# Performance work log

Hardware: AMD Instinct MI355X
Metric: run time of the kernel (lower is better)

The kernel has to match this reference:

```python
import jax, jax.numpy as jnp
import numpy as np

EMBED_DIM = 1024
NUM_HEADS = 16
HEAD_DIM = EMBED_DIM // NUM_HEADS
B, T = 4, 2048


def setup_inputs() -> dict:
    key = jax.random.key(0)
    ks = jax.random.split(key, 5)
    s = 0.02
    return {
        "x": jax.random.normal(ks[0], (B, T, EMBED_DIM), dtype=jnp.float32),
        "qkv_w": jax.random.normal(ks[1], (3 * EMBED_DIM, EMBED_DIM), dtype=jnp.float32) * s,
        "qkv_b": jax.random.normal(ks[2], (3 * EMBED_DIM,), dtype=jnp.float32) * s,
        "out_w": jax.random.normal(ks[3], (EMBED_DIM, EMBED_DIM), dtype=jnp.float32) * s,
        "out_b": jax.random.normal(ks[4], (EMBED_DIM,), dtype=jnp.float32) * s,
    }


def reference(x, qkv_w, qkv_b, out_w, out_b):
    b, t, c = x.shape
    h, d = NUM_HEADS, HEAD_DIM
    # qkv projection: Linear uses y = x @ W^T + b
    qkv = jnp.einsum("btc,fc->btf", x, qkv_w) + qkv_b  # [B,T,3C]
    q, k, v = jnp.split(qkv, 3, axis=-1)
    # [B, H, T, D]
    q = q.reshape(b, t, h, d).transpose(0, 2, 1, 3)
    k = k.reshape(b, t, h, d).transpose(0, 2, 1, 3)
    v = v.reshape(b, t, h, d).transpose(0, 2, 1, 3)
    scores = jnp.einsum("bhqd,bhkd->bhqk", q, k) / jnp.sqrt(jnp.float32(d))
    causal = jnp.tril(jnp.ones((t, t), dtype=bool))
    scores = jnp.where(causal, scores, -jnp.inf)
    attn = jax.nn.softmax(scores, axis=-1)
    o = jnp.einsum("bhqk,bhkd->bhqd", attn, v)
    o = o.transpose(0, 2, 1, 3).reshape(b, t, c)
    return jnp.einsum("btc,fc->btf", o, out_w) + out_b
```

## Files before the change

kernel.cpp:

```cpp
#include <hip/hip_runtime.h>
#include <hip/hip_bf16.h>
#include <math.h>

#define SEQ   2048
#define NTOK  8192
#define EMB   1024
#define QKVF  3072
#define QSCALE 0.18033688f

typedef __bf16 bf16;
typedef __bf16 bf16x8 __attribute__((ext_vector_type(8)));
typedef __bf16 bf16x4 __attribute__((ext_vector_type(4)));
typedef unsigned short u16x8 __attribute__((ext_vector_type(8)));
typedef float  f32x4  __attribute__((ext_vector_type(4)));

__device__ __forceinline__ void gload_lds16(const bf16* g, bf16* l) {
    __builtin_amdgcn_global_load_lds(
        (const __attribute__((address_space(1))) unsigned int*)g,
        (__attribute__((address_space(3))) unsigned int*)l,
        16, 0, 0);
}

__global__ __launch_bounds__(256) void cvt_f32_bf16(const float* __restrict__ in,
                                                    bf16* __restrict__ out, int n) {
    int i = (blockIdx.x * 256 + threadIdx.x) * 4;
    if (i >= n) return;
    float4 f = *reinterpret_cast<const float4*>(in + i);
    bf16x4 o;
    o[0] = (bf16)f.x; o[1] = (bf16)f.y; o[2] = (bf16)f.z; o[3] = (bf16)f.w;
    *reinterpret_cast<bf16x4*>(out + i) = o;
}

__global__ __launch_bounds__(256) void cvt_qkvw_bf16(const float* __restrict__ in,
                                                     bf16* __restrict__ out) {
    int i = (blockIdx.x * 256 + threadIdx.x) * 4;
    float4 f = *reinterpret_cast<const float4*>(in + i);
    const float s = (i < EMB * EMB) ? QSCALE : 1.f;
    bf16x4 o;
    o[0] = (bf16)(f.x * s); o[1] = (bf16)(f.y * s);
    o[2] = (bf16)(f.z * s); o[3] = (bf16)(f.w * s);
    *reinterpret_cast<bf16x4*>(out + i) = o;
}

template <bool BF16OUT>
__global__ __launch_bounds__(256) void gemm_bt(const bf16* __restrict__ A,
                                               const bf16* __restrict__ Bm,
                                               const float* __restrict__ bias,
                                               void* __restrict__ out,
                                               int M, int N, int K, int scale_cols) {
    __shared__ bf16 As[2][128 * 64];
    __shared__ bf16 Bs[2][128 * 64];

    const int nbx = N >> 7;
    const int q8  = (nbx * (M >> 7)) >> 3;
    const int swz = ((int)blockIdx.x & 7) * q8 + ((int)blockIdx.x >> 3);
    const int bx  = swz % nbx;
    const int by  = swz / nbx;

    const int tid  = threadIdx.x;
    const int lane = tid & 63;
    const int wv   = tid >> 6;
    const int wr   = wv >> 1, wc = wv & 1;
    const int lr   = lane & 15, hi = lane >> 4;
    const size_t brow = (size_t)by * 128;
    const size_t bcol = (size_t)bx * 128;

    const f32x4 fzero = {0.f, 0.f, 0.f, 0.f};
    f32x4 acc[4][4];
#pragma unroll
    for (int m = 0; m < 4; ++m)
#pragma unroll
        for (int n = 0; n < 4; ++n) acc[m][n] = fzero;

    const int r8 = tid >> 3;
    const int c8 = tid & 7;

#define STAGE(buf, kt) do {                                                     \
    _Pragma("unroll")                                                           \
    for (int i_ = 0; i_ < 4; ++i_) {                                            \
        const int row_ = i_ * 32 + r8;                                          \
        const int lin_ = i_ * 256 + tid;                                        \
        gload_lds16(A  + (brow + row_) * (size_t)K + (size_t)(kt) * 64 + c8*8,  \
                    &As[buf][lin_ * 8]);                                        \
        gload_lds16(Bm + (bcol + row_) * (size_t)K + (size_t)(kt) * 64 + c8*8,  \
                    &Bs[buf][lin_ * 8]);                                        \
    }                                                                           \
} while (0)

    const int NT = K >> 6;
    STAGE(0, 0);
    int cur = 0;

    for (int kt = 0; kt < NT; ++kt) {
        if (kt + 1 < NT) {
            STAGE(cur ^ 1, kt + 1);
            asm volatile("s_waitcnt vmcnt(8)" ::: "memory");
        } else {
            asm volatile("s_waitcnt vmcnt(0)" ::: "memory");
        }
        __builtin_amdgcn_s_barrier();

#pragma unroll
        for (int kk = 0; kk < 2; ++kk) {
            bf16x8 af[4], bfr[4];
#pragma unroll
            for (int m = 0; m < 4; ++m)
                af[m] = *reinterpret_cast<const bf16x8*>(
                    &As[cur][(wr * 64 + m * 16 + lr) * 64 + kk * 32 + hi * 8]);
#pragma unroll
            for (int n = 0; n < 4; ++n)
                bfr[n] = *reinterpret_cast<const bf16x8*>(
                    &Bs[cur][(wc * 64 + n * 16 + lr) * 64 + kk * 32 + hi * 8]);
#pragma unroll
            for (int m = 0; m < 4; ++m)
#pragma unroll
                for (int n = 0; n < 4; ++n)
                    acc[m][n] = __builtin_amdgcn_mfma_f32_16x16x32_bf16(
                        af[m], bfr[n], acc[m][n], 0, 0, 0);
        }

        asm volatile("s_waitcnt lgkmcnt(0)" ::: "memory");
        __builtin_amdgcn_s_barrier();
        cur ^= 1;
    }

#pragma unroll
    for (int m = 0; m < 4; ++m)
#pragma unroll
        for (int n = 0; n < 4; ++n)
#pragma unroll
            for (int r = 0; r < 4; ++r) {
                const size_t row = brow + wr * 64 + m * 16 + hi * 4 + r;
                const size_t col = bcol + wc * 64 + n * 16 + lr;
                const float bb = bias[col];
                const float v = acc[m][n][r] + (((int)col < scale_cols) ? bb * QSCALE : bb);
                if (BF16OUT)
                    ((bf16*)out)[row * (size_t)N + col] = (bf16)v;
                else
                    ((float*)out)[row * (size_t)N + col] = v;
            }
#undef STAGE
}

__global__ __launch_bounds__(256) void attn_kernel(const bf16* __restrict__ qkv,
                                                   bf16* __restrict__ o) {
    const int bid = blockIdx.x;
    const int qt  = 15 - (bid >> 6);
    const int bh  = bid & 63;
    const int h   = bh & 15;
    const int b   = bh >> 4;
    const int qbase = qt * 128;

    const int tid  = threadIdx.x;
    const int wv   = tid >> 6;
    const int lane = tid & 63;
    const int lr   = lane & 15, hi = lane >> 4;

    __shared__ bf16 Ks[64 * 64];
    __shared__ bf16 Vt[64 * 64];
    __shared__ bf16 Pl[4 * 32 * 64];

    char* Ksb = (char*)Ks;
    char* Vtb = (char*)Vt;
    char* Pb  = (char*)(Pl + wv * 2048);

    const size_t tokbase = (size_t)b * SEQ;

    bf16x8 aq[2][2];
#pragma unroll
    for (int qf = 0; qf < 2; ++qf) {
        const bf16* qg = qkv + (tokbase + qbase + wv * 32 + qf * 16 + lr) * (size_t)QKVF
                         + h * 64;
#pragma unroll
        for (int kk = 0; kk < 2; ++kk)
            aq[qf][kk] = *reinterpret_cast<const bf16x8*>(qg + kk * 32 + hi * 8);
    }

    const f32x4 fzero = {0.f, 0.f, 0.f, 0.f};
    f32x4 oacc[2][4];
#pragma unroll
    for (int qf = 0; qf < 2; ++qf)
#pragma unroll
        for (int n = 0; n < 4; ++n) oacc[qf][n] = fzero;
    float m_r[2] = {-__builtin_inff(), -__builtin_inff()};
    float l_r[2] = {0.f, 0.f};

    const int nkv = qt * 2 + 2;

    const int kp = tid >> 3;
    const int vc = tid & 7;

    for (int kt = 0; kt < nkv; ++kt) {
        const size_t kvrow = tokbase + (size_t)kt * 64;
        __syncthreads();

#pragma unroll
        for (int j = 0; j < 2; ++j) {
            const int kr = wv * 16 + j * 8 + (lane >> 3);
            const int cg = (lane & 7) ^ ((lane >> 3) & 7);
            gload_lds16(qkv + (kvrow + kr) * (size_t)QKVF + EMB + h * 64 + cg * 8,
                        &Ks[(wv * 16 + j * 8) * 64 + lane * 8]);
        }

        {
            const bf16* vg = qkv + (kvrow + 2 * kp) * (size_t)QKVF + 2 * EMB + h * 64 + vc * 8;
            u16x8 v0 = *reinterpret_cast<const u16x8*>(vg);
            u16x8 v1 = *reinterpret_cast<const u16x8*>(vg + QKVF);
#pragma unroll
            for (int jj = 0; jj < 8; ++jj) {
                const int d = vc * 8 + jj;
                const unsigned int pr = (unsigned int)v0[jj] | ((unsigned int)v1[jj] << 16);
                *(unsigned int*)(Vtb + d * 128 + ((4 * kp) ^ (vc << 4))) = pr;
            }
        }
        __syncthreads();

        f32x4 s[2][4];
#pragma unroll
        for (int qf = 0; qf < 2; ++qf)
#pragma unroll
            for (int ktile = 0; ktile < 4; ++ktile) s[qf][ktile] = fzero;
#pragma unroll
        for (int ktile = 0; ktile < 4; ++ktile)
#pragma unroll
            for (int kk = 0; kk < 2; ++kk) {
                const int kr = ktile * 16 + lr;
                bf16x8 ak = *reinterpret_cast<const bf16x8*>(
                    Ksb + kr * 128 + ((kk * 64 + hi * 16) ^ ((kr & 7) << 4)));
#pragma unroll
                for (int qf = 0; qf < 2; ++qf)
                    s[qf][ktile] = __builtin_amdgcn_mfma_f32_16x16x32_bf16(
                        ak, aq[qf][kk], s[qf][ktile], 0, 0, 0);
            }

#pragma unroll
        for (int qf = 0; qf < 2; ++qf) {
            if (kt * 64 + 63 > qbase + wv * 32 + qf * 16) {
                const int qglob = qbase + wv * 32 + qf * 16 + lr;
#pragma unroll
                for (int ktile = 0; ktile < 4; ++ktile) {
                    const int kg0 = kt * 64 + ktile * 16 + hi * 4;
#pragma unroll
                    for (int r = 0; r < 4; ++r)
                        if (kg0 + r > qglob) s[qf][ktile][r] = -__builtin_inff();
                }
            }
        }

#pragma unroll
        for (int qf = 0; qf < 2; ++qf) {
            float t4[4];
#pragma unroll
            for (int ktile = 0; ktile < 4; ++ktile)
                t4[ktile] = fmaxf(fmaxf(s[qf][ktile][0], s[qf][ktile][1]),
                                  fmaxf(s[qf][ktile][2], s[qf][ktile][3]));
            float tm = fmaxf(fmaxf(t4[0], t4[1]), fmaxf(t4[2], t4[3]));
            tm = fmaxf(tm, __shfl_xor(tm, 16));
            tm = fmaxf(tm, __shfl_xor(tm, 32));

            const float mn = fmaxf(m_r[qf], tm);
            const float sc = __builtin_amdgcn_exp2f(m_r[qf] - mn);
            m_r[qf] = mn;

            float s4[4];
#pragma unroll
            for (int ktile = 0; ktile < 4; ++ktile) {
                float p0 = __builtin_amdgcn_exp2f(s[qf][ktile][0] - mn);
                float p1 = __builtin_amdgcn_exp2f(s[qf][ktile][1] - mn);
                float p2 = __builtin_amdgcn_exp2f(s[qf][ktile][2] - mn);
                float p3 = __builtin_amdgcn_exp2f(s[qf][ktile][3] - mn);
                s[qf][ktile][0] = p0; s[qf][ktile][1] = p1;
                s[qf][ktile][2] = p2; s[qf][ktile][3] = p3;
                s4[ktile] = (p0 + p1) + (p2 + p3);
            }
            float ts = (s4[0] + s4[1]) + (s4[2] + s4[3]);
            ts += __shfl_xor(ts, 16);
            ts += __shfl_xor(ts, 32);
            l_r[qf] = l_r[qf] * sc + ts;

            float scb[4];
#pragma unroll
            for (int r = 0; r < 4; ++r) scb[r] = __shfl(sc, hi * 4 + r);
#pragma unroll
            for (int n = 0; n < 4; ++n)
#pragma unroll
                for (int r = 0; r < 4; ++r) oacc[qf][n][r] *= scb[r];

            const int q = qf * 16 + lr;
#pragma unroll
            for (int ktile = 0; ktile < 4; ++ktile) {
                bf16x4 p4;
#pragma unroll
                for (int r = 0; r < 4; ++r) p4[r] = (bf16)s[qf][ktile][r];
                *(bf16x4*)(Pb + q * 128 + ((ktile * 32 + hi * 8) ^ ((q & 7) << 4))) = p4;
            }
        }

#pragma unroll
        for (int kk = 0; kk < 2; ++kk) {
            bf16x8 ap[2];
#pragma unroll
            for (int qf = 0; qf < 2; ++qf) {
                const int q = qf * 16 + lr;
                ap[qf] = *reinterpret_cast<const bf16x8*>(
                    Pb + q * 128 + ((kk * 64 + hi * 16) ^ ((q & 7) << 4)));
            }
#pragma unroll
            for (int n = 0; n < 4; ++n) {
                const int d = n * 16 + lr;
                bf16x8 bv = *reinterpret_cast<const bf16x8*>(
                    Vtb + d * 128 + ((kk * 64 + hi * 16) ^ (((d >> 3) & 7) << 4)));
#pragma unroll
                for (int qf = 0; qf < 2; ++qf)
                    oacc[qf][n] = __builtin_amdgcn_mfma_f32_16x16x32_bf16(
                        ap[qf], bv, oacc[qf][n], 0, 0, 0);
            }
        }
    }

#pragma unroll
    for (int qf = 0; qf < 2; ++qf) {
        const float linv = 1.f / l_r[qf];
        float li[4];
#pragma unroll
        for (int r = 0; r < 4; ++r) li[r] = __shfl(linv, hi * 4 + r);
        bf16* og = o + (tokbase + qbase + wv * 32 + qf * 16) * (size_t)EMB + h * 64;
#pragma unroll
        for (int n = 0; n < 4; ++n)
#pragma unroll
            for (int r = 0; r < 4; ++r)
                og[(hi * 4 + r) * (size_t)EMB + n * 16 + lr] =
                    (bf16)(oacc[qf][n][r] * li[r]);
    }
}

extern "C" void kernel_launch(void* const* d_in, const int* in_sizes, int n_in,
                              void* d_out, int out_size, void* d_ws, size_t ws_size,
                              hipStream_t stream) {
    const float* x     = (const float*)d_in[0];
    const float* qkv_w = (const float*)d_in[1];
    const float* qkv_b = (const float*)d_in[2];
    const float* out_w = (const float*)d_in[3];
    const float* out_b = (const float*)d_in[4];
    float* out = (float*)d_out;

    char* ws = (char*)d_ws;
    bf16* x_bf    = (bf16*)(ws);
    bf16* qkvw_bf = (bf16*)(ws + 16777216);
    bf16* outw_bf = (bf16*)(ws + 23068672);
    bf16* qkv_bf  = (bf16*)(ws + 25165824);
    bf16* o_bf    = (bf16*)(ws + 75497472);

    cvt_f32_bf16<<<8192, 256, 0, stream>>>(x,     x_bf,    NTOK * EMB);
    cvt_qkvw_bf16<<<3072, 256, 0, stream>>>(qkv_w, qkvw_bf);
    cvt_f32_bf16<<<1024, 256, 0, stream>>>(out_w, outw_bf, EMB * EMB);

    gemm_bt<true><<<(QKVF / 128) * (NTOK / 128), 256, 0, stream>>>(
        x_bf, qkvw_bf, qkv_b, qkv_bf, NTOK, QKVF, EMB, EMB);

    attn_kernel<<<4 * 16 * (SEQ / 128), 256, 0, stream>>>(qkv_bf, o_bf);

    gemm_bt<false><<<(EMB / 128) * (NTOK / 128), 256, 0, stream>>>(
        o_bf, outw_bf, out_b, out, NTOK, EMB, EMB, 0);
}
```

Measured before the change: 292.7 us.

## Enlarge GEMM tiles to 8 waves, swizzle LDS, shrink attention query tiles, defer rescale

The GEMM becomes a templated 512-thread kernel with 128x256 or 256x128 tiles, an XOR-swizzled LDS layout that avoids bank conflicts, and raised wave priority around the MFMA block. The attention kernel now uses 64-query tiles with one 16-row fragment per wave, which doubles the block count for better balance across the causal triangle. It also skips the online-softmax rescale of the output accumulator when no row's max increases. Larger GEMM tiles cut operand refetch but use more LDS and registers per block. Smaller attention tiles mean each K/V tile loaded into LDS is reused by fewer queries.

```diff
diff --git a/kernel.cpp b/kernel.cpp
--- a/kernel.cpp
+++ b/kernel.cpp
@@ -42,28 +42,30 @@
     *reinterpret_cast<bf16x4*>(out + i) = o;
 }
 
-template <bool BF16OUT>
-__global__ __launch_bounds__(256) void gemm_bt(const bf16* __restrict__ A,
-                                               const bf16* __restrict__ Bm,
-                                               const float* __restrict__ bias,
-                                               void* __restrict__ out,
-                                               int M, int N, int K, int scale_cols) {
-    __shared__ bf16 As[2][128 * 64];
-    __shared__ bf16 Bs[2][128 * 64];
-
-    const int nbx = N >> 7;
-    const int q8  = (nbx * (M >> 7)) >> 3;
+template <int WR, int WC, bool BF16OUT>
+__global__ __launch_bounds__(512, 2) void gemm_bt8(const bf16* __restrict__ A,
+                                                   const bf16* __restrict__ Bm,
+                                                   const float* __restrict__ bias,
+                                                   void* __restrict__ out,
+                                                   int M, int N, int K, int scale_cols) {
+    constexpr int BM = WR * 64, BN = WC * 64;
+    constexpr int WN = WR + WC;
+    __shared__ bf16 As[2][BM * 64];
+    __shared__ bf16 Bs[2][BN * 64];
+
+    const int nbx = N / BN;
+    const int q8  = (nbx * (M / BM)) >> 3;
     const int swz = ((int)blockIdx.x & 7) * q8 + ((int)blockIdx.x >> 3);
     const int bx  = swz % nbx;
     const int by  = swz / nbx;
 
     const int tid  = threadIdx.x;
     const int lane = tid & 63;
-    const int wv   = tid >> 6;
-    const int wr   = wv >> 1, wc = wv & 1;
+    const int wid  = tid >> 6;
+    const int wr   = wid / WC, wc = wid % WC;
     const int lr   = lane & 15, hi = lane >> 4;
-    const size_t brow = (size_t)by * 128;
-    const size_t bcol = (size_t)bx * 128;
+    const size_t brow = (size_t)by * BM;
+    const size_t bcol = (size_t)bx * BN;
 
     const f32x4 fzero = {0.f, 0.f, 0.f, 0.f};
     f32x4 acc[4][4];
@@ -77,13 +79,18 @@
 
 #define STAGE(buf, kt) do {                                                     \
     _Pragma("unroll")                                                           \
-    for (int i_ = 0; i_ < 4; ++i_) {                                            \
-        const int row_ = i_ * 32 + r8;                                          \
-        const int lin_ = i_ * 256 + tid;                                        \
-        gload_lds16(A  + (brow + row_) * (size_t)K + (size_t)(kt) * 64 + c8*8,  \
-                    &As[buf][lin_ * 8]);                                        \
-        gload_lds16(Bm + (bcol + row_) * (size_t)K + (size_t)(kt) * 64 + c8*8,  \
-                    &Bs[buf][lin_ * 8]);                                        \
+    for (int i_ = 0; i_ < WR; ++i_) {                                           \
+        const int row_ = i_ * 64 + r8;                                          \
+        const int cg_  = c8 ^ (row_ & 7);                                       \
+        gload_lds16(A + (brow + row_) * (size_t)K + (size_t)(kt) * 64 + cg_*8,  \
+                    &As[buf][i_ * 4096 + tid * 8]);                             \
+    }                                                                           \
+    _Pragma("unroll")                                                           \
+    for (int i_ = 0; i_ < WC; ++i_) {                                           \
+        const int row_ = i_ * 64 + r8;                                          \
+        const int cg_  = c8 ^ (row_ & 7);                                       \
+        gload_lds16(Bm + (bcol + row_) * (size_t)K + (size_t)(kt) * 64 + cg_*8, \
+                    &Bs[buf][i_ * 4096 + tid * 8]);                             \
     }                                                                           \
 } while (0)
 
@@ -94,7 +101,7 @@
     for (int kt = 0; kt < NT; ++kt) {
         if (kt + 1 < NT) {
             STAGE(cur ^ 1, kt + 1);
-            asm volatile("s_waitcnt vmcnt(8)" ::: "memory");
+            asm volatile("s_waitcnt vmcnt(%0)" :: "i"(WN) : "memory");
         } else {
             asm volatile("s_waitcnt vmcnt(0)" ::: "memory");
         }
@@ -104,19 +111,27 @@
         for (int kk = 0; kk < 2; ++kk) {
             bf16x8 af[4], bfr[4];
 #pragma unroll
-            for (int m = 0; m < 4; ++m)
+            for (int m = 0; m < 4; ++m) {
+                const int row = wr * 64 + m * 16 + lr;
                 af[m] = *reinterpret_cast<const bf16x8*>(
-                    &As[cur][(wr * 64 + m * 16 + lr) * 64 + kk * 32 + hi * 8]);
-#pragma unroll
-            for (int n = 0; n < 4; ++n)
+                    (const char*)&As[cur][0] + row * 128 +
+                    ((kk * 64 + hi * 16) ^ ((row & 7) << 4)));
+            }
+#pragma unroll
+            for (int n = 0; n < 4; ++n) {
+                const int row = wc * 64 + n * 16 + lr;
                 bfr[n] = *reinterpret_cast<const bf16x8*>(
-                    &Bs[cur][(wc * 64 + n * 16 + lr) * 64 + kk * 32 + hi * 8]);
+                    (const char*)&Bs[cur][0] + row * 128 +
+                    ((kk * 64 + hi * 16) ^ ((row & 7) << 4)));
+            }
+            __builtin_amdgcn_s_setprio(1);
 #pragma unroll
             for (int m = 0; m < 4; ++m)
 #pragma unroll
                 for (int n = 0; n < 4; ++n)
                     acc[m][n] = __builtin_amdgcn_mfma_f32_16x16x32_bf16(
                         af[m], bfr[n], acc[m][n], 0, 0, 0);
+            __builtin_amdgcn_s_setprio(0);
         }
 
         asm volatile("s_waitcnt lgkmcnt(0)" ::: "memory");
@@ -145,11 +160,11 @@
 __global__ __launch_bounds__(256) void attn_kernel(const bf16* __restrict__ qkv,
                                                    bf16* __restrict__ o) {
     const int bid = blockIdx.x;
-    const int qt  = 15 - (bid >> 6);
+    const int qt  = 31 - (bid >> 6);
     const int bh  = bid & 63;
     const int h   = bh & 15;
     const int b   = bh >> 4;
-    const int qbase = qt * 128;
+    const int qbase = qt * 64;
 
     const int tid  = threadIdx.x;
     const int wv   = tid >> 6;
@@ -158,34 +173,28 @@
 
     __shared__ bf16 Ks[64 * 64];
     __shared__ bf16 Vt[64 * 64];
-    __shared__ bf16 Pl[4 * 32 * 64];
+    __shared__ bf16 Pl[4 * 16 * 64];
 
     char* Ksb = (char*)Ks;
     char* Vtb = (char*)Vt;
-    char* Pb  = (char*)(Pl + wv * 2048);
+    char* Pb  = (char*)(Pl + wv * 1024);
 
     const size_t tokbase = (size_t)b * SEQ;
 
-    bf16x8 aq[2][2];
-#pragma unroll
-    for (int qf = 0; qf < 2; ++qf) {
-        const bf16* qg = qkv + (tokbase + qbase + wv * 32 + qf * 16 + lr) * (size_t)QKVF
-                         + h * 64;
-#pragma unroll
-        for (int kk = 0; kk < 2; ++kk)
-            aq[qf][kk] = *reinterpret_cast<const bf16x8*>(qg + kk * 32 + hi * 8);
-    }
+    const bf16* qg = qkv + (tokbase + qbase + wv * 16 + lr) * (size_t)QKVF + h * 64;
+    bf16x8 aq[2];
+#pragma unroll
+    for (int kk = 0; kk < 2; ++kk)
+        aq[kk] = *reinterpret_cast<const bf16x8*>(qg + kk * 32 + hi * 8);
 
     const f32x4 fzero = {0.f, 0.f, 0.f, 0.f};
-    f32x4 oacc[2][4];
-#pragma unroll
-    for (int qf = 0; qf < 2; ++qf)
-#pragma unroll
-        for (int n = 0; n < 4; ++n) oacc[qf][n] = fzero;
-    float m_r[2] = {-__builtin_inff(), -__builtin_inff()};
-    float l_r[2] = {0.f, 0.f};
-
-    const int nkv = qt * 2 + 2;
+    f32x4 oacc[4];
+#pragma unroll
+    for (int n = 0; n < 4; ++n) oacc[n] = fzero;
+    float m_r = -__builtin_inff();
+    float l_r = 0.f;
+
+    const int nkv = qt + 1;
 
     const int kp = tid >> 3;
     const int vc = tid & 7;
@@ -215,11 +224,9 @@
         }
         __syncthreads();
 
-        f32x4 s[2][4];
-#pragma unroll
-        for (int qf = 0; qf < 2; ++qf)
-#pragma unroll
-            for (int ktile = 0; ktile < 4; ++ktile) s[qf][ktile] = fzero;
+        f32x4 s[4];
+#pragma unroll
+        for (int ktile = 0; ktile < 4; ++ktile) s[ktile] = fzero;
 #pragma unroll
         for (int ktile = 0; ktile < 4; ++ktile)
 #pragma unroll
@@ -227,110 +234,102 @@
                 const int kr = ktile * 16 + lr;
                 bf16x8 ak = *reinterpret_cast<const bf16x8*>(
                     Ksb + kr * 128 + ((kk * 64 + hi * 16) ^ ((kr & 7) << 4)));
-#pragma unroll
-                for (int qf = 0; qf < 2; ++qf)
-                    s[qf][ktile] = __builtin_amdgcn_mfma_f32_16x16x32_bf16(
-                        ak, aq[qf][kk], s[qf][ktile], 0, 0, 0);
-            }
-
-#pragma unroll
-        for (int qf = 0; qf < 2; ++qf) {
-            if (kt * 64 + 63 > qbase + wv * 32 + qf * 16) {
-                const int qglob = qbase + wv * 32 + qf * 16 + lr;
-#pragma unroll
-                for (int ktile = 0; ktile < 4; ++ktile) {
-                    const int kg0 = kt * 64 + ktile * 16 + hi * 4;
-#pragma unroll
-                    for (int r = 0; r < 4; ++r)
-                        if (kg0 + r > qglob) s[qf][ktile][r] = -__builtin_inff();
-                }
-            }
-        }
-
-#pragma unroll
-        for (int qf = 0; qf < 2; ++qf) {
+                s[ktile] = __builtin_amdgcn_mfma_f32_16x16x32_bf16(
+                    ak, aq[kk], s[ktile], 0, 0, 0);
+            }
+
+        if (kt * 64 + 63 > qbase + wv * 16) {
+            const int qglob = qbase + wv * 16 + lr;
+#pragma unroll
+            for (int ktile = 0; ktile < 4; ++ktile) {
+                const int kg0 = kt * 64 + ktile * 16 + hi * 4;
+#pragma unroll
+                for (int r = 0; r < 4; ++r)
+                    if (kg0 + r > qglob) s[ktile][r] = -__builtin_inff();
+            }
+        }
+
+        {
             float t4[4];
 #pragma unroll
             for (int ktile = 0; ktile < 4; ++ktile)
-                t4[ktile] = fmaxf(fmaxf(s[qf][ktile][0], s[qf][ktile][1]),
-                                  fmaxf(s[qf][ktile][2], s[qf][ktile][3]));
+                t4[ktile] = fmaxf(fmaxf(s[ktile][0], s[ktile][1]),
+                                  fmaxf(s[ktile][2], s[ktile][3]));
             float tm = fmaxf(fmaxf(t4[0], t4[1]), fmaxf(t4[2], t4[3]));
             tm = fmaxf(tm, __shfl_xor(tm, 16));
             tm = fmaxf(tm, __shfl_xor(tm, 32));
 
-            const float mn = fmaxf(m_r[qf], tm);
-            const float sc = __builtin_amdgcn_exp2f(m_r[qf] - mn);
-            m_r[qf] = mn;
+            const bool defer = __all(tm <= m_r);
+            const float mn = defer ? m_r : fmaxf(m_r, tm);
 
             float s4[4];
 #pragma unroll
             for (int ktile = 0; ktile < 4; ++ktile) {
-                float p0 = __builtin_amdgcn_exp2f(s[qf][ktile][0] - mn);
-                float p1 = __builtin_amdgcn_exp2f(s[qf][ktile][1] - mn);
-                float p2 = __builtin_amdgcn_exp2f(s[qf][ktile][2] - mn);
-                float p3 = __builtin_amdgcn_exp2f(s[qf][ktile][3] - mn);
-                s[qf][ktile][0] = p0; s[qf][ktile][1] = p1;
-                s[qf][ktile][2] = p2; s[qf][ktile][3] = p3;
+                float p0 = __builtin_amdgcn_exp2f(s[ktile][0] - mn);
+                float p1 = __builtin_amdgcn_exp2f(s[ktile][1] - mn);
+                float p2 = __builtin_amdgcn_exp2f(s[ktile][2] - mn);
+                float p3 = __builtin_amdgcn_exp2f(s[ktile][3] - mn);
+                s[ktile][0] = p0; s[ktile][1] = p1;
+                s[ktile][2] = p2; s[ktile][3] = p3;
                 s4[ktile] = (p0 + p1) + (p2 + p3);
             }
             float ts = (s4[0] + s4[1]) + (s4[2] + s4[3]);
             ts += __shfl_xor(ts, 16);
             ts += __shfl_xor(ts, 32);
-            l_r[qf] = l_r[qf] * sc + ts;
-
-            float scb[4];
-#pragma unroll
-            for (int r = 0; r < 4; ++r) scb[r] = __shfl(sc, hi * 4 + r);
-#pragma unroll
-            for (int n = 0; n < 4; ++n)
-#pragma unroll
-                for (int r = 0; r < 4; ++r) oacc[qf][n][r] *= scb[r];
-
-            const int q = qf * 16 + lr;
+
+            if (defer) {
+                l_r += ts;
+            } else {
+                const float sc = __builtin_amdgcn_exp2f(m_r - mn);
+                m_r = mn;
+                l_r = l_r * sc + ts;
+                float scb[4];
+#pragma unroll
+                for (int r = 0; r < 4; ++r) scb[r] = __shfl(sc, hi * 4 + r);
+#pragma unroll
+                for (int n = 0; n < 4; ++n)
+#pragma unroll
+                    for (int r = 0; r < 4; ++r) oacc[n][r] *= scb[r];
+            }
+
+            const int q = lr;
 #pragma unroll
             for (int ktile = 0; ktile < 4; ++ktile) {
                 bf16x4 p4;
 #pragma unroll
-                for (int r = 0; r < 4; ++r) p4[r] = (bf16)s[qf][ktile][r];
+                for (int r = 0; r < 4; ++r) p4[r] = (bf16)s[ktile][r];
                 *(bf16x4*)(Pb + q * 128 + ((ktile * 32 + hi * 8) ^ ((q & 7) << 4))) = p4;
             }
         }
 
 #pragma unroll
         for (int kk = 0; kk < 2; ++kk) {
-            bf16x8 ap[2];
-#pragma unroll
-            for (int qf = 0; qf < 2; ++qf) {
-                const int q = qf * 16 + lr;
-                ap[qf] = *reinterpret_cast<const bf16x8*>(
-                    Pb + q * 128 + ((kk * 64 + hi * 16) ^ ((q & 7) << 4)));
-            }
+            const int q = lr;
+            bf16x8 ap = *reinterpret_cast<const bf16x8*>(
+                Pb + q * 128 + ((kk * 64 + hi * 16) ^ ((q & 7) << 4)));
 #pragma unroll
             for (int n = 0; n < 4; ++n) {
                 const int d = n * 16 + lr;
                 bf16x8 bv = *reinterpret_cast<const bf16x8*>(
                     Vtb + d * 128 + ((kk * 64 + hi * 16) ^ (((d >> 3) & 7) << 4)));
-#pragma unroll
-                for (int qf = 0; qf < 2; ++qf)
-                    oacc[qf][n] = __builtin_amdgcn_mfma_f32_16x16x32_bf16(
-                        ap[qf], bv, oacc[qf][n], 0, 0, 0);
+                oacc[n] = __builtin_amdgcn_mfma_f32_16x16x32_bf16(
+                    ap, bv, oacc[n], 0, 0, 0);
             }
         }
     }
 
-#pragma unroll
-    for (int qf = 0; qf < 2; ++qf) {
-        const float linv = 1.f / l_r[qf];
+    {
+        const float linv = 1.f / l_r;
         float li[4];
 #pragma unroll
         for (int r = 0; r < 4; ++r) li[r] = __shfl(linv, hi * 4 + r);
-        bf16* og = o + (tokbase + qbase + wv * 32 + qf * 16) * (size_t)EMB + h * 64;
+        bf16* og = o + (tokbase + qbase + wv * 16) * (size_t)EMB + h * 64;
 #pragma unroll
         for (int n = 0; n < 4; ++n)
 #pragma unroll
             for (int r = 0; r < 4; ++r)
                 og[(hi * 4 + r) * (size_t)EMB + n * 16 + lr] =
-                    (bf16)(oacc[qf][n][r] * li[r]);
+                    (bf16)(oacc[n][r] * li[r]);
     }
 }
 
@@ -355,11 +354,11 @@
     cvt_qkvw_bf16<<<3072, 256, 0, stream>>>(qkv_w, qkvw_bf);
     cvt_f32_bf16<<<1024, 256, 0, stream>>>(out_w, outw_bf, EMB * EMB);
 
-    gemm_bt<true><<<(QKVF / 128) * (NTOK / 128), 256, 0, stream>>>(
+    gemm_bt8<2, 4, true><<<(NTOK / 128) * (QKVF / 256), 512, 0, stream>>>(
         x_bf, qkvw_bf, qkv_b, qkv_bf, NTOK, QKVF, EMB, EMB);
 
-    attn_kernel<<<4 * 16 * (SEQ / 128), 256, 0, stream>>>(qkv_bf, o_bf);
-
-    gemm_bt<false><<<(EMB / 128) * (NTOK / 128), 256, 0, stream>>>(
+    attn_kernel<<<4 * 16 * (SEQ / 64), 256, 0, stream>>>(qkv_bf, o_bf);
+
+    gemm_bt8<4, 2, false><<<(NTOK / 256) * (EMB / 128), 512, 0, stream>>>(
         o_bf, outw_bf, out_b, out, NTOK, EMB, EMB, 0);
 }
```

Measured after the change: 288.1 us. About the same (-1.6%).

## Enlarge GEMM tiles with 8 waves, swizzle LDS, pipeline attention K/V loads, defer rescale

Applied to the files above, without the earlier changes.

The GEMMs move to 512-thread blocks with 128x256 or 256x128 tiles, an XOR-swizzled LDS layout to avoid bank conflicts, and raised priority around the MFMA blocks. The attention kernel double-buffers K in LDS and prefetches V into registers for the next tile, cutting one barrier per iteration. It also skips the output rescale when the running max does not change across the wave. The aim is better data reuse and latency hiding, at the cost of more LDS and register pressure, which may lower occupancy.

```diff
diff --git a/kernel.cpp b/kernel.cpp
--- a/kernel.cpp
+++ b/kernel.cpp
@@ -42,28 +42,30 @@
     *reinterpret_cast<bf16x4*>(out + i) = o;
 }
 
-template <bool BF16OUT>
-__global__ __launch_bounds__(256) void gemm_bt(const bf16* __restrict__ A,
-                                               const bf16* __restrict__ Bm,
-                                               const float* __restrict__ bias,
-                                               void* __restrict__ out,
-                                               int M, int N, int K, int scale_cols) {
-    __shared__ bf16 As[2][128 * 64];
-    __shared__ bf16 Bs[2][128 * 64];
-
-    const int nbx = N >> 7;
-    const int q8  = (nbx * (M >> 7)) >> 3;
+template <int WR, int WC, bool BF16OUT>
+__global__ __launch_bounds__(512, 2) void gemm_bt8(const bf16* __restrict__ A,
+                                                   const bf16* __restrict__ Bm,
+                                                   const float* __restrict__ bias,
+                                                   void* __restrict__ out,
+                                                   int M, int N, int K, int scale_cols) {
+    constexpr int BM = WR * 64, BN = WC * 64;
+    constexpr int WN = WR + WC;
+    __shared__ bf16 As[2][BM * 64];
+    __shared__ bf16 Bs[2][BN * 64];
+
+    const int nbx = N / BN;
+    const int q8  = (nbx * (M / BM)) >> 3;
     const int swz = ((int)blockIdx.x & 7) * q8 + ((int)blockIdx.x >> 3);
     const int bx  = swz % nbx;
     const int by  = swz / nbx;
 
     const int tid  = threadIdx.x;
     const int lane = tid & 63;
-    const int wv   = tid >> 6;
-    const int wr   = wv >> 1, wc = wv & 1;
+    const int wid  = tid >> 6;
+    const int wr   = wid / WC, wc = wid % WC;
     const int lr   = lane & 15, hi = lane >> 4;
-    const size_t brow = (size_t)by * 128;
-    const size_t bcol = (size_t)bx * 128;
+    const size_t brow = (size_t)by * BM;
+    const size_t bcol = (size_t)bx * BN;
 
     const f32x4 fzero = {0.f, 0.f, 0.f, 0.f};
     f32x4 acc[4][4];
@@ -77,13 +79,18 @@
 
 #define STAGE(buf, kt) do {                                                     \
     _Pragma("unroll")                                                           \
-    for (int i_ = 0; i_ < 4; ++i_) {                                            \
-        const int row_ = i_ * 32 + r8;                                          \
-        const int lin_ = i_ * 256 + tid;                                        \
-        gload_lds16(A  + (brow + row_) * (size_t)K + (size_t)(kt) * 64 + c8*8,  \
-                    &As[buf][lin_ * 8]);                                        \
-        gload_lds16(Bm + (bcol + row_) * (size_t)K + (size_t)(kt) * 64 + c8*8,  \
-                    &Bs[buf][lin_ * 8]);                                        \
+    for (int i_ = 0; i_ < WR; ++i_) {                                           \
+        const int row_ = i_ * 64 + r8;                                          \
+        const int cg_  = c8 ^ (row_ & 7);                                       \
+        gload_lds16(A + (brow + row_) * (size_t)K + (size_t)(kt) * 64 + cg_*8,  \
+                    &As[buf][i_ * 4096 + tid * 8]);                             \
+    }                                                                           \
+    _Pragma("unroll")                                                           \
+    for (int i_ = 0; i_ < WC; ++i_) {                                           \
+        const int row_ = i_ * 64 + r8;                                          \
+        const int cg_  = c8 ^ (row_ & 7);                                       \
+        gload_lds16(Bm + (bcol + row_) * (size_t)K + (size_t)(kt) * 64 + cg_*8, \
+                    &Bs[buf][i_ * 4096 + tid * 8]);                             \
     }                                                                           \
 } while (0)
 
@@ -94,7 +101,7 @@
     for (int kt = 0; kt < NT; ++kt) {
         if (kt + 1 < NT) {
             STAGE(cur ^ 1, kt + 1);
-            asm volatile("s_waitcnt vmcnt(8)" ::: "memory");
+            asm volatile("s_waitcnt vmcnt(%0)" :: "i"(WN) : "memory");
         } else {
             asm volatile("s_waitcnt vmcnt(0)" ::: "memory");
         }
@@ -104,19 +111,27 @@
         for (int kk = 0; kk < 2; ++kk) {
             bf16x8 af[4], bfr[4];
 #pragma unroll
-            for (int m = 0; m < 4; ++m)
+            for (int m = 0; m < 4; ++m) {
+                const int row = wr * 64 + m * 16 + lr;
                 af[m] = *reinterpret_cast<const bf16x8*>(
-                    &As[cur][(wr * 64 + m * 16 + lr) * 64 + kk * 32 + hi * 8]);
-#pragma unroll
-            for (int n = 0; n < 4; ++n)
+                    (const char*)&As[cur][0] + row * 128 +
+                    ((kk * 64 + hi * 16) ^ ((row & 7) << 4)));
+            }
+#pragma unroll
+            for (int n = 0; n < 4; ++n) {
+                const int row = wc * 64 + n * 16 + lr;
                 bfr[n] = *reinterpret_cast<const bf16x8*>(
-                    &Bs[cur][(wc * 64 + n * 16 + lr) * 64 + kk * 32 + hi * 8]);
+                    (const char*)&Bs[cur][0] + row * 128 +
+                    ((kk * 64 + hi * 16) ^ ((row & 7) << 4)));
+            }
+            __builtin_amdgcn_s_setprio(1);
 #pragma unroll
             for (int m = 0; m < 4; ++m)
 #pragma unroll
                 for (int n = 0; n < 4; ++n)
                     acc[m][n] = __builtin_amdgcn_mfma_f32_16x16x32_bf16(
                         af[m], bfr[n], acc[m][n], 0, 0, 0);
+            __builtin_amdgcn_s_setprio(0);
         }
 
         asm volatile("s_waitcnt lgkmcnt(0)" ::: "memory");
@@ -142,8 +157,8 @@
 #undef STAGE
 }
 
-__global__ __launch_bounds__(256) void attn_kernel(const bf16* __restrict__ qkv,
-                                                   bf16* __restrict__ o) {
+__global__ __launch_bounds__(256, 4) void attn_kernel(const bf16* __restrict__ qkv,
+                                                      bf16* __restrict__ o) {
     const int bid = blockIdx.x;
     const int qt  = 15 - (bid >> 6);
     const int bh  = bid & 63;
@@ -156,11 +171,10 @@
     const int lane = tid & 63;
     const int lr   = lane & 15, hi = lane >> 4;
 
-    __shared__ bf16 Ks[64 * 64];
+    __shared__ bf16 Ks[2][64 * 64];
     __shared__ bf16 Vt[64 * 64];
     __shared__ bf16 Pl[4 * 32 * 64];
 
-    char* Ksb = (char*)Ks;
     char* Vtb = (char*)Vt;
     char* Pb  = (char*)(Pl + wv * 2048);
 
@@ -189,31 +203,49 @@
 
     const int kp = tid >> 3;
     const int vc = tid & 7;
+    const int kr8 = lane >> 3;
+    const int kc8 = (lane & 7) ^ ((lane >> 3) & 7);
+
+#define STAGE_K(dst, kvrow) do {                                                 \
+    _Pragma("unroll")                                                            \
+    for (int j_ = 0; j_ < 2; ++j_) {                                             \
+        const int kr_ = wv * 16 + j_ * 8 + kr8;                                  \
+        gload_lds16(qkv + ((kvrow) + kr_) * (size_t)QKVF + EMB + h * 64 + kc8*8, \
+                    &(dst)[(wv * 16 + j_ * 8) * 64 + lane * 8]);                 \
+    }                                                                            \
+} while (0)
+#define LOAD_V(kvrow, v0_, v1_) do {                                             \
+    const bf16* vg_ = qkv + ((kvrow) + 2 * kp) * (size_t)QKVF + 2 * EMB + h * 64 \
+                      + vc * 8;                                                  \
+    v0_ = *reinterpret_cast<const u16x8*>(vg_);                                  \
+    v1_ = *reinterpret_cast<const u16x8*>(vg_ + QKVF);                           \
+} while (0)
+
+    STAGE_K(Ks[0], tokbase);
+    u16x8 nv0, nv1;
+    LOAD_V(tokbase, nv0, nv1);
 
     for (int kt = 0; kt < nkv; ++kt) {
-        const size_t kvrow = tokbase + (size_t)kt * 64;
+        const char* Ksb = (const char*)Ks[kt & 1];
+
         __syncthreads();
 
 #pragma unroll
-        for (int j = 0; j < 2; ++j) {
-            const int kr = wv * 16 + j * 8 + (lane >> 3);
-            const int cg = (lane & 7) ^ ((lane >> 3) & 7);
-            gload_lds16(qkv + (kvrow + kr) * (size_t)QKVF + EMB + h * 64 + cg * 8,
-                        &Ks[(wv * 16 + j * 8) * 64 + lane * 8]);
-        }
-
-        {
-            const bf16* vg = qkv + (kvrow + 2 * kp) * (size_t)QKVF + 2 * EMB + h * 64 + vc * 8;
-            u16x8 v0 = *reinterpret_cast<const u16x8*>(vg);
-            u16x8 v1 = *reinterpret_cast<const u16x8*>(vg + QKVF);
-#pragma unroll
-            for (int jj = 0; jj < 8; ++jj) {
-                const int d = vc * 8 + jj;
-                const unsigned int pr = (unsigned int)v0[jj] | ((unsigned int)v1[jj] << 16);
-                *(unsigned int*)(Vtb + d * 128 + ((4 * kp) ^ (vc << 4))) = pr;
-            }
-        }
-        __syncthreads();
+        for (int jj = 0; jj < 8; ++jj) {
+            const int d = vc * 8 + jj;
+            const unsigned int pr = (unsigned int)nv0[jj] | ((unsigned int)nv1[jj] << 16);
+            *(unsigned int*)(Vtb + d * 128 + ((4 * kp) ^ (vc << 4))) = pr;
+        }
+
+        if (kt + 1 < nkv)
+            STAGE_K(Ks[(kt + 1) & 1], tokbase + (size_t)(kt + 1) * 64);
+
+        asm volatile("s_waitcnt lgkmcnt(0)" ::: "memory");
+        __builtin_amdgcn_s_barrier();
+        __builtin_amdgcn_sched_barrier(0);
+
+        if (kt + 1 < nkv)
+            LOAD_V(tokbase + (size_t)(kt + 1) * 64, nv0, nv1);
 
         f32x4 s[2][4];
 #pragma unroll
@@ -258,9 +290,8 @@
             tm = fmaxf(tm, __shfl_xor(tm, 16));
             tm = fmaxf(tm, __shfl_xor(tm, 32));
 
-            const float mn = fmaxf(m_r[qf], tm);
-            const float sc = __builtin_amdgcn_exp2f(m_r[qf] - mn);
-            m_r[qf] = mn;
+            const bool defer = __all(tm <= m_r[qf]);
+            const float mn = defer ? m_r[qf] : fmaxf(m_r[qf], tm);
 
             float s4[4];
 #pragma unroll
@@ -276,15 +307,21 @@
             float ts = (s4[0] + s4[1]) + (s4[2] + s4[3]);
             ts += __shfl_xor(ts, 16);
             ts += __shfl_xor(ts, 32);
-            l_r[qf] = l_r[qf] * sc + ts;
-
-            float scb[4];
-#pragma unroll
-            for (int r = 0; r < 4; ++r) scb[r] = __shfl(sc, hi * 4 + r);
-#pragma unroll
-            for (int n = 0; n < 4; ++n)
-#pragma unroll
-                for (int r = 0; r < 4; ++r) oacc[qf][n][r] *= scb[r];
+
+            if (defer) {
+                l_r[qf] += ts;
+            } else {
+                const float sc = __builtin_amdgcn_exp2f(m_r[qf] - mn);
+                m_r[qf] = mn;
+                l_r[qf] = l_r[qf] * sc + ts;
+                float scb[4];
+#pragma unroll
+                for (int r = 0; r < 4; ++r) scb[r] = __shfl(sc, hi * 4 + r);
+#pragma unroll
+                for (int n = 0; n < 4; ++n)
+#pragma unroll
+                    for (int r = 0; r < 4; ++r) oacc[qf][n][r] *= scb[r];
+            }
 
             const int q = qf * 16 + lr;
 #pragma unroll
@@ -332,6 +369,8 @@
                 og[(hi * 4 + r) * (size_t)EMB + n * 16 + lr] =
                     (bf16)(oacc[qf][n][r] * li[r]);
     }
+#undef STAGE_K
+#undef LOAD_V
 }
 
 extern "C" void kernel_launch(void* const* d_in, const int* in_sizes, int n_in,
@@ -355,11 +394,11 @@
     cvt_qkvw_bf16<<<3072, 256, 0, stream>>>(qkv_w, qkvw_bf);
     cvt_f32_bf16<<<1024, 256, 0, stream>>>(out_w, outw_bf, EMB * EMB);
 
-    gemm_bt<true><<<(QKVF / 128) * (NTOK / 128), 256, 0, stream>>>(
+    gemm_bt8<2, 4, true><<<(NTOK / 128) * (QKVF / 256), 512, 0, stream>>>(
         x_bf, qkvw_bf, qkv_b, qkv_bf, NTOK, QKVF, EMB, EMB);
 
     attn_kernel<<<4 * 16 * (SEQ / 128), 256, 0, stream>>>(qkv_bf, o_bf);
 
-    gemm_bt<false><<<(EMB / 128) * (NTOK / 128), 256, 0, stream>>>(
+    gemm_bt8<4, 2, false><<<(NTOK / 256) * (EMB / 128), 512, 0, stream>>>(
         o_bf, outw_bf, out_b, out, NTOK, EMB, EMB, 0);
 }
```

Result: no change. 293.6 us (+0.3%).
